# Optimization experiments

Measured on AMD Instinct MI355X. Metric: run time of the kernel, lower is better.

## Reference

```python
import jax, jax.numpy as jnp
import numpy as np

VS = VT = 32000; E = 512; H = 512; B = 32; S = 128; T = 128


def _gru_step(x, h, Wx, bx, Urz, brz, Un, bn):
    # x: [B, I], h: [B, H]
    gx = x @ Wx + bx                       # [B, 3H]
    xr, xz, xn = jnp.split(gx, 3, axis=-1)
    hrz = h @ Urz + brz                    # [B, 2H]
    hr, hz = jnp.split(hrz, 2, axis=-1)
    r = jax.nn.sigmoid(xr + hr)
    z = jax.nn.sigmoid(xz + hz)
    n = jnp.tanh(xn + (r * h) @ Un + bn)
    return (1.0 - z) * h + z * n


def setup_inputs() -> dict:
    key = jax.random.key(0)
    ks = jax.random.split(key, 24)
    s = 0.02
    f = lambda k, shape: (jax.random.normal(k, shape, dtype=jnp.float32) * s)
    return {
        "src": jax.random.randint(ks[0], (B, S), 0, VS),
        "tgt": jax.random.randint(ks[1], (B, T), 0, VT),
        "enc_embed": f(ks[2], (VS, E)),
        "enc_Wx": f(ks[3], (E, 3 * H)),
        "enc_bx": jnp.zeros((3 * H,), jnp.float32),
        "enc_Urz": f(ks[4], (H, 2 * H)),
        "enc_brz": jnp.zeros((2 * H,), jnp.float32),
        "enc_Un": f(ks[5], (H, H)),
        "enc_bn": jnp.zeros((H,), jnp.float32),
        "dec_embed": f(ks[6], (VT, E)),
        "dec_Wx": f(ks[7], (E + H, 3 * H)),
        "dec_bx": jnp.zeros((3 * H,), jnp.float32),
        "dec_Urz": f(ks[8], (H, 2 * H)),
        "dec_brz": jnp.zeros((2 * H,), jnp.float32),
        "dec_Un": f(ks[9], (H, H)),
        "dec_bn": jnp.zeros((H,), jnp.float32),
        "attn_Wh": f(ks[10], (H, H)),
        "attn_Ws": f(ks[11], (H, H)),
        "attn_v": f(ks[12], (H,)),
        "out_W": f(ks[13], (2 * H, VT)),
        "out_b": jnp.zeros((VT,), jnp.float32),
    }


def reference(src, tgt, enc_embed, enc_Wx, enc_bx, enc_Urz, enc_brz, enc_Un,
              enc_bn, dec_embed, dec_Wx, dec_bx, dec_Urz, dec_brz, dec_Un,
              dec_bn, attn_Wh, attn_Ws, attn_v, out_W, out_b):
    bs = src.shape[0]
    h0 = jnp.zeros((bs, H), dtype=enc_Wx.dtype)

    # -------- encoder: scan over src timesteps --------
    src_emb = enc_embed[src]                     # [B, S, E]

    def enc_step(h, x_t):
        h = _gru_step(x_t, h, enc_Wx, enc_bx, enc_Urz, enc_brz, enc_Un, enc_bn)
        return h, h

    h, enc_hs = jax.lax.scan(enc_step, h0, jnp.swapaxes(src_emb, 0, 1))
    enc_hs = jnp.swapaxes(enc_hs, 0, 1)          # [B, S, H]

    # precompute Wh(enc_hs), identical every decoder step
    wh_enc = enc_hs @ attn_Wh                    # [B, S, H]

    # -------- decoder: scan over tgt timesteps --------
    tgt_emb = dec_embed[tgt]                     # [B, T, E]

    def dec_step(h, emb_t):
        # Bahdanau attention
        energy = jnp.einsum('bsh,h->bs', jnp.tanh(wh_enc + (h @ attn_Ws)[:, None, :]), attn_v)
        attn = jax.nn.softmax(energy, axis=-1)   # [B, S]
        ctx = jnp.einsum('bs,bsh->bh', attn, enc_hs)
        x = jnp.concatenate([emb_t, ctx], axis=-1)   # [B, E+H]
        h = _gru_step(x, h, dec_Wx, dec_bx, dec_Urz, dec_brz, dec_Un, dec_bn)
        logits = jnp.concatenate([h, ctx], axis=-1) @ out_W + out_b
        out = jax.nn.log_softmax(logits, axis=-1)
        return h, out

    _, outputs = jax.lax.scan(dec_step, h, jnp.swapaxes(tgt_emb, 0, 1))
    return jnp.swapaxes(outputs, 0, 1)           # [B, T, VT]
```

## Files before the change

kernel.cpp:

```cpp
#include <hip/hip_runtime.h>
#include <stdint.h>

#define BATCH 32
#define SEQ   128
#define HID   512
#define VTOK  32000

typedef unsigned short u16;
typedef unsigned int   u32;
typedef unsigned long long u64;
typedef float    f32x4  __attribute__((ext_vector_type(4)));
typedef short    short8 __attribute__((ext_vector_type(8)));

__device__ __forceinline__ u16 f2bf(float f) {
    u32 u = __builtin_bit_cast(u32, f);
    return (u16)((u + 0x7FFFu + ((u >> 16) & 1u)) >> 16);
}
__device__ __forceinline__ float bf2f(u16 v) {
    u32 u = ((u32)v) << 16; return __builtin_bit_cast(float, u);
}
__device__ __forceinline__ float fexp2(float x) { return __builtin_amdgcn_exp2f(x); }
__device__ __forceinline__ float frcp(float x)  { return __builtin_amdgcn_rcpf(x); }
__device__ __forceinline__ float sigmoid_f(float x) {
    return frcp(1.f + fexp2(-1.442695040888963f * x));
}
__device__ __forceinline__ float tanh_f(float x) {
    return 1.f - 2.f * frcp(1.f + fexp2(2.885390081777927f * x));
}

__device__ __forceinline__ u32 ld_sc1_u32(const u32* p) {
    return __hip_atomic_load(p, __ATOMIC_RELAXED, __HIP_MEMORY_SCOPE_AGENT);
}
__device__ __forceinline__ void st_sc1_u32(u32* p, u32 v) {
    __hip_atomic_store(p, v, __ATOMIC_RELAXED, __HIP_MEMORY_SCOPE_AGENT);
}

__device__ __forceinline__ void ld16_async(uint4& dst, const void* p) {
    asm volatile("global_load_dwordx4 %0, %1, off sc1" : "=v"(dst) : "v"(p));
}
__device__ __forceinline__ void ld4_async(u32& dst, const void* p) {
    asm volatile("global_load_dword %0, %1, off sc1" : "=v"(dst) : "v"(p));
}
__device__ __forceinline__ void wait_vm0() {
    asm volatile("s_waitcnt vmcnt(0)" ::: "memory");
    __builtin_amdgcn_sched_barrier(0);
}

__device__ __forceinline__ void gbar32(u32* flags, u32 gen) {
    asm volatile("s_waitcnt vmcnt(0)" ::: "memory");
    __syncthreads();
    if (threadIdx.x == 0) st_sc1_u32(flags + (u32)blockIdx.x * 16, gen);
    const int i = threadIdx.x;
    if (i < 32 && i != (int)blockIdx.x) {
        while (ld_sc1_u32(flags + i * 16) < gen) {}
    }
    __syncthreads();
}


__global__ __launch_bounds__(256) void transpose_cvt(
    const float* __restrict__ src, u16* __restrict__ dst, int K, int N)
{
    __shared__ float tile[32][33];
    const int n0 = blockIdx.x * 32, k0 = blockIdx.y * 32;
    const int tx = threadIdx.x & 31, ty = threadIdx.x >> 5;
    #pragma unroll
    for (int j = 0; j < 32; j += 8)
        tile[ty + j][tx] = src[(size_t)(k0 + ty + j) * N + n0 + tx];
    __syncthreads();
    #pragma unroll
    for (int j = 0; j < 32; j += 8)
        dst[(size_t)(n0 + ty + j) * K + k0 + tx] = f2bf(tile[tx][ty + j]);
}

__global__ __launch_bounds__(256) void cvt_f32_bf16(
    const float* __restrict__ src, u16* __restrict__ dst)
{
    const size_t i = ((size_t)blockIdx.x * 256 + threadIdx.x) * 8;
    float4 v0 = *(const float4*)(src + i);
    float4 v1 = *(const float4*)(src + i + 4);
    uint4 pk;
    pk.x = (u32)f2bf(v0.x) | ((u32)f2bf(v0.y) << 16);
    pk.y = (u32)f2bf(v0.z) | ((u32)f2bf(v0.w) << 16);
    pk.z = (u32)f2bf(v1.x) | ((u32)f2bf(v1.y) << 16);
    pk.w = (u32)f2bf(v1.z) | ((u32)f2bf(v1.w) << 16);
    *(uint4*)(dst + i) = pk;
}

__global__ __launch_bounds__(128) void gather_emb_bf16(
    const int* __restrict__ idx, const float* __restrict__ emb, u16* __restrict__ out)
{
    const int r = blockIdx.x;
    const int token = idx[r];
    const int i = threadIdx.x * 4;
    float4 v = *(const float4*)(emb + (size_t)token * 512 + i);
    uint2 pk;
    pk.x = (u32)f2bf(v.x) | ((u32)f2bf(v.y) << 16);
    pk.y = (u32)f2bf(v.z) | ((u32)f2bf(v.w) << 16);
    *(uint2*)(out + (size_t)r * 512 + i) = pk;
}

__global__ __launch_bounds__(512) void init_state(u32* hg, u32* bar)
{
    const int i = blockIdx.x * 512 + threadIdx.x;
    hg[i] = 0u;
    if (blockIdx.x < 2) bar[blockIdx.x * 512 + threadIdx.x] = 0u;
}

__global__ __launch_bounds__(256) void gemm_bf16(
    const u16* __restrict__ A, const u16* __restrict__ BT,
    const float* __restrict__ bias, float* __restrict__ C,
    int M, int N, int K)
{
    __shared__ __align__(16) u16 As[128][40];
    __shared__ __align__(16) u16 Bs[128][40];
    const int tid  = threadIdx.x;
    const int lane = tid & 63, wave = tid >> 6;
    const int wm = (wave & 1) * 64, wn = (wave >> 1) * 64;
    const int lrow = lane & 15, lk = (lane >> 4) * 8;
    const int srow = tid >> 2, skof = (tid & 3) * 8;
    const size_t K_ = (size_t)K;
    const u16* Ag = A + ((size_t)blockIdx.y * 128 + srow) * K_ + skof;
    const u16* Bg = BT + ((size_t)blockIdx.x * 128 + srow) * K_ + skof;
    f32x4 acc[4][4] = {};
    for (int k0 = 0; k0 < K; k0 += 32) {
        uint4 a0 = *(const uint4*)(Ag + k0);
        uint4 a1 = *(const uint4*)(Ag + 64 * K_ + k0);
        uint4 b0 = *(const uint4*)(Bg + k0);
        uint4 b1 = *(const uint4*)(Bg + 64 * K_ + k0);
        __syncthreads();
        *(uint4*)&As[srow][skof]      = a0;
        *(uint4*)&As[srow + 64][skof] = a1;
        *(uint4*)&Bs[srow][skof]      = b0;
        *(uint4*)&Bs[srow + 64][skof] = b1;
        __syncthreads();
        short8 af[4], bf[4];
        #pragma unroll
        for (int i = 0; i < 4; ++i) af[i] = *(const short8*)&As[wm + i * 16 + lrow][lk];
        #pragma unroll
        for (int j = 0; j < 4; ++j) bf[j] = *(const short8*)&Bs[wn + j * 16 + lrow][lk];
        #pragma unroll
        for (int i = 0; i < 4; ++i)
            #pragma unroll
            for (int j = 0; j < 4; ++j)
                acc[i][j] = __builtin_amdgcn_mfma_f32_16x16x32_bf16(af[i], bf[j], acc[i][j], 0, 0, 0);
    }
    const int crow0 = blockIdx.y * 128 + wm + (lane >> 4) * 4;
    const int ccol0 = blockIdx.x * 128 + wn + (lane & 15);
    #pragma unroll
    for (int j = 0; j < 4; ++j) {
        const float bv = bias ? bias[ccol0 + j * 16] : 0.f;
        #pragma unroll
        for (int i = 0; i < 4; ++i)
            #pragma unroll
            for (int rr = 0; rr < 4; ++rr)
                C[(size_t)(crow0 + i * 16 + rr) * N + (ccol0 + j * 16)] = acc[i][j][rr] + bv;
    }
}

__global__ __launch_bounds__(512) void enc_coop(
    const float* __restrict__ gx, const u16* __restrict__ Urz, const u16* __restrict__ Un,
    const float* __restrict__ brz, const float* __restrict__ bn,
    u32* __restrict__ hg, u32* __restrict__ rhg, u32* __restrict__ zg,
    u16* __restrict__ enc_hs, u16* __restrict__ spack,
    u32* __restrict__ flags)
{
    const int w = blockIdx.x, tid = threadIdx.x;
    const int v = tid >> 6, lane = tid & 63;
    const int nl = lane & 15, kq = lane >> 4;
    __shared__ __align__(16) u16 UrzS[32][520];
    __shared__ __align__(16) u16 UnS[16][520];
    for (int idx = tid; idx < 32 * 64; idx += 512) {
        const int r = idx >> 6, c = idx & 63;
        *(uint4*)&UrzS[r][c * 8] = *(const uint4*)(Urz + (size_t)(w * 32 + r) * 512 + c * 8);
    }
    for (int idx = tid; idx < 16 * 64; idx += 512) {
        const int r = idx >> 6, c = idx & 63;
        *(uint4*)&UnS[r][c * 8] = *(const uint4*)(Un + (size_t)(w * 16 + r) * 512 + c * 8);
    }
    __syncthreads();
    for (int t = 0; t < SEQ; ++t) {
        const u32* hgA = hg + (t & 1) * 8192;
        u32*       hgW = hg + ((t + 1) & 1) * 8192;
        const u64* hq  = (const u64*)hgA;
        const u64* rq  = (const u64*)rhg;
        if (v < 4) {
            const int bt = v & 1, tl = v >> 1;
            const int n = w * 32 + tl * 16 + nl;
            const int brow = bt * 16 + nl;
            uint4 a[16]; u32 hvp[4];
            const u64* ab = hq + brow * 128 + kq * 2;
            #pragma unroll
            for (int i = 0; i < 16; ++i) ld16_async(a[i], ab + i * 8);
            #pragma unroll
            for (int rr = 0; rr < 4; ++rr)
                ld4_async(hvp[rr], hgA + (bt * 16 + kq * 4 + rr) * 256 + (n >> 1));
            float gxr_pf[4];
            #pragma unroll
            for (int rr = 0; rr < 4; ++rr) {
                const int b = bt * 16 + kq * 4 + rr;
                gxr_pf[rr] = gx[((size_t)(b * SEQ + t)) * 1536 + n];
            }
            wait_vm0();
            const u16* wl = &UrzS[tl * 16 + nl][0];
            f32x4 acc = {0.f, 0.f, 0.f, 0.f};
            #pragma unroll
            for (int i = 0; i < 16; ++i) {
                short8 bfv = *(const short8*)(wl + i * 32 + kq * 8);
                acc = __builtin_amdgcn_mfma_f32_16x16x32_bf16(
                    __builtin_bit_cast(short8, a[i]), bfv, acc, 0, 0, 0);
            }
            if (n < 512) {
                u32 pk[4];
                #pragma unroll
                for (int rr = 0; rr < 4; ++rr) {
                    const float r = sigmoid_f(gxr_pf[rr] + acc[rr] + brz[n]);
                    const float hold = bf2f((u16)((n & 1) ? (hvp[rr] >> 16) : (hvp[rr] & 0xFFFF)));
                    pk[rr] = (u32)f2bf(r * hold);
                }
                #pragma unroll
                for (int rr = 0; rr < 4; ++rr) {
                    u32 oth = (u32)__shfl_xor((int)pk[rr], 1);
                    if ((n & 1) == 0) {
                        const int b = bt * 16 + kq * 4 + rr;
                        st_sc1_u32(rhg + b * 256 + (n >> 1), (pk[rr] & 0xFFFF) | (oth << 16));
                    }
                }
            } else {
                #pragma unroll
                for (int rr = 0; rr < 4; ++rr) {
                    const int b = bt * 16 + kq * 4 + rr;
                    const float z = sigmoid_f(gxr_pf[rr] + acc[rr] + brz[n]);
                    st_sc1_u32(zg + b * 512 + (n - 512), __float_as_uint(z));
                }
            }
        }
        gbar32(flags, (u32)(2 * t + 1));
        if (v < 2) {
            const int bt = v;
            const int n = w * 16 + nl;
            const int brow = bt * 16 + nl;
            uint4 a[16]; u32 hvp[4], zvp[4];
            const u64* ab = rq + brow * 128 + kq * 2;
            #pragma unroll
            for (int i = 0; i < 16; ++i) ld16_async(a[i], ab + i * 8);
            #pragma unroll
            for (int rr = 0; rr < 4; ++rr) {
                const int b = bt * 16 + kq * 4 + rr;
                ld4_async(hvp[rr], hgA + b * 256 + (n >> 1));
                ld4_async(zvp[rr], zg + b * 512 + n);
            }
            float gxr_pf[4];
            #pragma unroll
            for (int rr = 0; rr < 4; ++rr) {
                const int b = bt * 16 + kq * 4 + rr;
                gxr_pf[rr] = gx[((size_t)(b * SEQ + t)) * 1536 + 1024 + n];
            }
            wait_vm0();
            const u16* wl = &UnS[nl][0];
            f32x4 acc = {0.f, 0.f, 0.f, 0.f};
            #pragma unroll
            for (int i = 0; i < 16; ++i) {
                short8 bfv = *(const short8*)(wl + i * 32 + kq * 8);
                acc = __builtin_amdgcn_mfma_f32_16x16x32_bf16(
                    __builtin_bit_cast(short8, a[i]), bfv, acc, 0, 0, 0);
            }
            u32 pk[4];
            #pragma unroll
            for (int rr = 0; rr < 4; ++rr) {
                const int b = bt * 16 + kq * 4 + rr;
                const float nn = tanh_f(gxr_pf[rr] + acc[rr] + bn[n]);
                const float z = __uint_as_float(zvp[rr]);
                const float hold = bf2f((u16)((n & 1) ? (hvp[rr] >> 16) : (hvp[rr] & 0xFFFF)));
                const float hn = (1.f - z) * hold + z * nn;
                const u16 hb = f2bf(hn);
                pk[rr] = (u32)hb;
                enc_hs[((size_t)(b * SEQ + t)) * 512 + n] = hb;
                spack[(((size_t)b * 16 + (t >> 3)) * 512 + n) * 8 + (t & 7)] = hb;
            }
            #pragma unroll
            for (int rr = 0; rr < 4; ++rr) {
                u32 oth = (u32)__shfl_xor((int)pk[rr], 1);
                if ((n & 1) == 0) {
                    const int b = bt * 16 + kq * 4 + rr;
                    st_sc1_u32(hgW + b * 256 + (n >> 1), (pk[rr] & 0xFFFF) | (oth << 16));
                }
            }
        }
        gbar32(flags, (u32)(2 * t + 2));
    }
}

__global__ __launch_bounds__(512) void dec_coop(
    const float* __restrict__ gxe, const u16* __restrict__ wh_bf, const u16* __restrict__ spack,
    const float* __restrict__ attn_v, const float* __restrict__ brz, const float* __restrict__ bn,
    const u16* __restrict__ Urz, const u16* __restrict__ Ws,
    const u16* __restrict__ WxC, const u16* __restrict__ Un,
    u32* __restrict__ hg, u32* __restrict__ rhg, u32* __restrict__ ctxg,
    u32* __restrict__ zg, u32* __restrict__ gg, u32* __restrict__ aWsg,
    u16* __restrict__ hctx, u32* __restrict__ flags)
{
    const int w = blockIdx.x, tid = threadIdx.x;
    const int v = tid >> 6, lane = tid & 63;
    const int nl = lane & 15, kq = lane >> 4;
    __shared__ __align__(16) u16 UWsS[48][520];
    __shared__ __align__(16) u16 WxCS[48][520];
    __shared__ __align__(16) u16 UnS2[16][520];
    __shared__ float hWsL[4 * 132], redE[512], attnL[128];
    __shared__ u16 ctxL[512];
    for (int idx = tid; idx < 48 * 64; idx += 512) {
        const int r = idx >> 6, c = idx & 63;
        const int gcol = w * 48 + r;
        const u16* s0 = (gcol < 1024 ? Urz + (size_t)gcol * 512
                                     : Ws + (size_t)(gcol - 1024) * 512) + c * 8;
        *(uint4*)&UWsS[r][c * 8] = *(const uint4*)s0;
        *(uint4*)&WxCS[r][c * 8] = *(const uint4*)(WxC + (size_t)gcol * 512 + c * 8);
    }
    for (int idx = tid; idx < 16 * 64; idx += 512) {
        const int r = idx >> 6, c = idx & 63;
        *(uint4*)&UnS2[r][c * 8] = *(const uint4*)(Un + (size_t)(w * 16 + r) * 512 + c * 8);
    }
    __syncthreads();
    for (int t = 0; t < SEQ; ++t) {
        const u32* hgA = hg + (t & 1) * 8192;
        u32*       hgW = hg + ((t + 1) & 1) * 8192;
        const u64* hq  = (const u64*)hgA;
        const u64* rq  = (const u64*)rhg;
        const u64* cq  = (const u64*)ctxg;
        f32x4 aPk = {0.f, 0.f, 0.f, 0.f};
        if (v < 6) {
            const int bt = v & 1, tl = v >> 1;
            const int n = w * 48 + tl * 16 + nl;
            const int brow = bt * 16 + nl;
            uint4 a[16];
            const u64* ab = hq + brow * 128 + kq * 2;
            #pragma unroll
            for (int i = 0; i < 16; ++i) ld16_async(a[i], ab + i * 8);
            wait_vm0();
            const u16* wl = &UWsS[tl * 16 + nl][0];
            f32x4 acc = {0.f, 0.f, 0.f, 0.f};
            #pragma unroll
            for (int i = 0; i < 16; ++i) {
                short8 bfv = *(const short8*)(wl + i * 32 + kq * 8);
                acc = __builtin_amdgcn_mfma_f32_16x16x32_bf16(
                    __builtin_bit_cast(short8, a[i]), bfv, acc, 0, 0, 0);
            }
            if (n < 1024) {
                aPk = acc;
            } else {
                #pragma unroll
                for (int rr = 0; rr < 4; ++rr) {
                    const int b = bt * 16 + kq * 4 + rr;
                    st_sc1_u32(aWsg + b * 512 + (n - 1024), __float_as_uint(acc[rr]));
                }
            }
        }
        gbar32(flags, (u32)(4 * t + 1));
        {
            const int b = w;
            {
                u32 hwv;
                ld4_async(hwv, aWsg + b * 512 + tid);
                wait_vm0();
                hWsL[(tid >> 7) * 132 + (tid & 127)] = __uint_as_float(hwv);
            }
            __syncthreads();
            {
                const int s = tid >> 2, q = tid & 3;
                const u16* whr = wh_bf + ((size_t)(b * SEQ + s)) * 512 + q * 128;
                const float* avq = attn_v + q * 128;
                const float* hwq = &hWsL[q * 132];
                float e = 0.f;
                #pragma unroll 4
                for (int i = 0; i < 128; i += 8) {
                    uint4 wv = *(const uint4*)(whr + i);
                    float4 h0 = *(const float4*)(hwq + i);
                    float4 h1 = *(const float4*)(hwq + i + 4);
                    float4 v0 = *(const float4*)(avq + i);
                    float4 v1 = *(const float4*)(avq + i + 4);
                    e += v0.x * tanh_f(bf2f((u16)(wv.x & 0xFFFF)) + h0.x)
                       + v0.y * tanh_f(bf2f((u16)(wv.x >> 16))    + h0.y)
                       + v0.z * tanh_f(bf2f((u16)(wv.y & 0xFFFF)) + h0.z)
                       + v0.w * tanh_f(bf2f((u16)(wv.y >> 16))    + h0.w)
                       + v1.x * tanh_f(bf2f((u16)(wv.z & 0xFFFF)) + h1.x)
                       + v1.y * tanh_f(bf2f((u16)(wv.z >> 16))    + h1.y)
                       + v1.z * tanh_f(bf2f((u16)(wv.w & 0xFFFF)) + h1.z)
                       + v1.w * tanh_f(bf2f((u16)(wv.w >> 16))    + h1.w);
                }
                redE[tid] = e;
            }
            __syncthreads();
            if (tid < 64) {
                float e0 = redE[4 * tid] + redE[4 * tid + 1] + redE[4 * tid + 2] + redE[4 * tid + 3];
                float e1 = redE[4 * (tid + 64)] + redE[4 * (tid + 64) + 1]
                         + redE[4 * (tid + 64) + 2] + redE[4 * (tid + 64) + 3];
                float m = fmaxf(e0, e1);
                for (int o = 32; o >= 1; o >>= 1) m = fmaxf(m, __shfl_xor(m, o));
                float p0 = fexp2((e0 - m) * 1.442695040888963f);
                float p1 = fexp2((e1 - m) * 1.442695040888963f);
                float ss = p0 + p1;
                for (int o = 32; o >= 1; o >>= 1) ss += __shfl_xor(ss, o);
                const float inv = frcp(ss);
                attnL[tid]      = p0 * inv;
                attnL[tid + 64] = p1 * inv;
            }
            __syncthreads();
            {
                const int d = tid;
                float cv = 0.f;
                const u16* sp = spack + ((size_t)b * 16 * 512 + d) * 8;
                #pragma unroll 4
                for (int sb = 0; sb < 16; ++sb) {
                    uint4 sv = *(const uint4*)(sp + (size_t)sb * 4096);
                    const float* al = &attnL[sb * 8];
                    cv += al[0] * bf2f((u16)(sv.x & 0xFFFF)) + al[1] * bf2f((u16)(sv.x >> 16))
                        + al[2] * bf2f((u16)(sv.y & 0xFFFF)) + al[3] * bf2f((u16)(sv.y >> 16))
                        + al[4] * bf2f((u16)(sv.z & 0xFFFF)) + al[5] * bf2f((u16)(sv.z >> 16))
                        + al[6] * bf2f((u16)(sv.w & 0xFFFF)) + al[7] * bf2f((u16)(sv.w >> 16));
                }
                const u16 cb = f2bf(cv);
                ctxL[d] = cb;
                hctx[((size_t)(b * SEQ + t)) * 1024 + 512 + d] = cb;
            }
            __syncthreads();
            if (tid < 256) {
                u32 pk = (u32)ctxL[2 * tid] | ((u32)ctxL[2 * tid + 1] << 16);
                st_sc1_u32(ctxg + b * 256 + tid, pk);
            }
        }
        gbar32(flags, (u32)(4 * t + 2));
        if (v < 6) {
            const int bt = v & 1, tl = v >> 1;
            const int n = w * 48 + tl * 16 + nl;
            const int brow = bt * 16 + nl;
            uint4 a[16]; u32 hvp[4];
            const u64* ab = cq + brow * 128 + kq * 2;
            #pragma unroll
            for (int i = 0; i < 16; ++i) ld16_async(a[i], ab + i * 8);
            #pragma unroll
            for (int rr = 0; rr < 4; ++rr)
                ld4_async(hvp[rr], hgA + (bt * 16 + kq * 4 + rr) * 256 + ((n & 511) >> 1));
            float gxr_pf[4];
            #pragma unroll
            for (int rr = 0; rr < 4; ++rr) {
                const int b = bt * 16 + kq * 4 + rr;
                gxr_pf[rr] = gxe[((size_t)(b * SEQ + t)) * 1536 + n];
            }
            wait_vm0();
            const u16* wl = &WxCS[tl * 16 + nl][0];
            f32x4 acc = {0.f, 0.f, 0.f, 0.f};
            #pragma unroll
            for (int i = 0; i < 16; ++i) {
                short8 bfv = *(const short8*)(wl + i * 32 + kq * 8);
                acc = __builtin_amdgcn_mfma_f32_16x16x32_bf16(
                    __builtin_bit_cast(short8, a[i]), bfv, acc, 0, 0, 0);
            }
            if (n < 512) {
                u32 pk[4];
                #pragma unroll
                for (int rr = 0; rr < 4; ++rr) {
                    const float r = sigmoid_f(gxr_pf[rr] + acc[rr] + aPk[rr] + brz[n]);
                    const float hold = bf2f((u16)((n & 1) ? (hvp[rr] >> 16) : (hvp[rr] & 0xFFFF)));
                    pk[rr] = (u32)f2bf(r * hold);
                }
                #pragma unroll
                for (int rr = 0; rr < 4; ++rr) {
                    u32 oth = (u32)__shfl_xor((int)pk[rr], 1);
                    if ((n & 1) == 0) {
                        const int b = bt * 16 + kq * 4 + rr;
                        st_sc1_u32(rhg + b * 256 + (n >> 1), (pk[rr] & 0xFFFF) | (oth << 16));
                    }
                }
            } else if (n < 1024) {
                #pragma unroll
                for (int rr = 0; rr < 4; ++rr) {
                    const int b = bt * 16 + kq * 4 + rr;
                    const float z = sigmoid_f(gxr_pf[rr] + acc[rr] + aPk[rr] + brz[n]);
                    st_sc1_u32(zg + b * 512 + (n - 512), __float_as_uint(z));
                }
            } else {
                #pragma unroll
                for (int rr = 0; rr < 4; ++rr) {
                    const int b = bt * 16 + kq * 4 + rr;
                    st_sc1_u32(gg + b * 512 + (n - 1024), __float_as_uint(gxr_pf[rr] + acc[rr]));
                }
            }
        }
        gbar32(flags, (u32)(4 * t + 3));
        if (v < 2) {
            const int bt = v;
            const int n = w * 16 + nl;
            const int brow = bt * 16 + nl;
            uint4 a[16]; u32 gvp[4], zvp[4], hvp[4];
            const u64* ab = rq + brow * 128 + kq * 2;
            #pragma unroll
            for (int i = 0; i < 16; ++i) ld16_async(a[i], ab + i * 8);
            #pragma unroll
            for (int rr = 0; rr < 4; ++rr) {
                const int b = bt * 16 + kq * 4 + rr;
                ld4_async(gvp[rr], gg + b * 512 + n);
                ld4_async(zvp[rr], zg + b * 512 + n);
                ld4_async(hvp[rr], hgA + b * 256 + (n >> 1));
            }
            wait_vm0();
            const u16* wl = &UnS2[nl][0];
            f32x4 acc = {0.f, 0.f, 0.f, 0.f};
            #pragma unroll
            for (int i = 0; i < 16; ++i) {
                short8 bfv = *(const short8*)(wl + i * 32 + kq * 8);
                acc = __builtin_amdgcn_mfma_f32_16x16x32_bf16(
                    __builtin_bit_cast(short8, a[i]), bfv, acc, 0, 0, 0);
            }
            u32 pk[4];
            #pragma unroll
            for (int rr = 0; rr < 4; ++rr) {
                const int b = bt * 16 + kq * 4 + rr;
                const float nn = tanh_f(__uint_as_float(gvp[rr]) + acc[rr] + bn[n]);
                const float z = __uint_as_float(zvp[rr]);
                const float hold = bf2f((u16)((n & 1) ? (hvp[rr] >> 16) : (hvp[rr] & 0xFFFF)));
                const float hn = (1.f - z) * hold + z * nn;
                const u16 hb = f2bf(hn);
                pk[rr] = (u32)hb;
                hctx[((size_t)(b * SEQ + t)) * 1024 + n] = hb;
            }
            #pragma unroll
            for (int rr = 0; rr < 4; ++rr) {
                u32 oth = (u32)__shfl_xor((int)pk[rr], 1);
                if ((n & 1) == 0) {
                    const int b = bt * 16 + kq * 4 + rr;
                    st_sc1_u32(hgW + b * 256 + (n >> 1), (pk[rr] & 0xFFFF) | (oth << 16));
                }
            }
        }
        gbar32(flags, (u32)(4 * t + 4));
    }
}

__global__ __launch_bounds__(256) void log_softmax_rows(float* __restrict__ out)
{
    const int row = blockIdx.x, tid = threadIdx.x;
    float* p = out + (size_t)row * VTOK;
    __shared__ float rbM[4], rbS[4];
    const float L2E = 1.442695040888963f;
    float m = -3.0e38f, s = 0.f;
    for (int i = tid * 4; i < VTOK; i += 1024) {
        float4 v = *(const float4*)(p + i);
        float lm = fmaxf(fmaxf(v.x, v.y), fmaxf(v.z, v.w));
        float nm = fmaxf(m, lm);
        s = s * fexp2((m - nm) * L2E)
          + fexp2((v.x - nm) * L2E) + fexp2((v.y - nm) * L2E)
          + fexp2((v.z - nm) * L2E) + fexp2((v.w - nm) * L2E);
        m = nm;
    }
    for (int o = 32; o >= 1; o >>= 1) {
        float om = __shfl_xor(m, o), os = __shfl_xor(s, o);
        float nm = fmaxf(m, om);
        s = s * fexp2((m - nm) * L2E) + os * fexp2((om - nm) * L2E);
        m = nm;
    }
    if ((tid & 63) == 0) { rbM[tid >> 6] = m; rbS[tid >> 6] = s; }
    __syncthreads();
    {
        float fm = fmaxf(fmaxf(rbM[0], rbM[1]), fmaxf(rbM[2], rbM[3]));
        float fs = rbS[0] * fexp2((rbM[0] - fm) * L2E) + rbS[1] * fexp2((rbM[1] - fm) * L2E)
                 + rbS[2] * fexp2((rbM[2] - fm) * L2E) + rbS[3] * fexp2((rbM[3] - fm) * L2E);
        m = fm; s = fs;
    }
    const float lse = m + __builtin_amdgcn_logf(s) * 0.6931471805599453f;
    for (int i = tid * 4; i < VTOK; i += 1024) {
        float4 v = *(const float4*)(p + i);
        v.x -= lse; v.y -= lse; v.z -= lse; v.w -= lse;
        *(float4*)(p + i) = v;
    }
}

extern "C" void kernel_launch(void* const* d_in, const int* in_sizes, int n_in,
                              void* d_out, int out_size, void* d_ws, size_t ws_size,
                              hipStream_t stream)
{
    (void)in_sizes; (void)n_in; (void)out_size; (void)ws_size;
    const int*   src       = (const int*)  d_in[0];
    const int*   tgt       = (const int*)  d_in[1];
    const float* enc_embed = (const float*)d_in[2];
    const float* enc_Wx    = (const float*)d_in[3];
    const float* enc_bx    = (const float*)d_in[4];
    const float* enc_Urz   = (const float*)d_in[5];
    const float* enc_brz   = (const float*)d_in[6];
    const float* enc_Un    = (const float*)d_in[7];
    const float* enc_bn    = (const float*)d_in[8];
    const float* dec_embed = (const float*)d_in[9];
    const float* dec_Wx    = (const float*)d_in[10];
    const float* dec_bx    = (const float*)d_in[11];
    const float* dec_Urz   = (const float*)d_in[12];
    const float* dec_brz   = (const float*)d_in[13];
    const float* dec_Un    = (const float*)d_in[14];
    const float* dec_bn    = (const float*)d_in[15];
    const float* attn_Wh   = (const float*)d_in[16];
    const float* attn_Ws   = (const float*)d_in[17];
    const float* attn_v    = (const float*)d_in[18];
    const float* out_W     = (const float*)d_in[19];
    const float* out_b     = (const float*)d_in[20];

    char* ob = (char*)d_out;
    float* gx_enc   = (float*)(ob + 0);
    float* gxe_dec  = (float*)(ob + 25165824);
    float* wh_enc   = (float*)(ob + 50331648);
    u16*   Aenc     = (u16*)(ob + 58720256);
    u16*   Adec     = (u16*)(ob + 62914560);
    u16*   enc_hs   = (u16*)(ob + 67108864);
    u16*   spack    = (u16*)(ob + 71303168);
    u16*   wh_bf    = (u16*)(ob + 75497472);
    u16*   encWxT   = (u16*)(ob + 79691776);
    u16*   decWxET  = (u16*)(ob + 81264640);
    u16*   WhT      = (u16*)(ob + 82837504);
    u16*   UrzET    = (u16*)(ob + 83361792);
    u16*   UnET     = (u16*)(ob + 84410368);
    u16*   UrzDT    = (u16*)(ob + 84934656);
    u16*   UnDT     = (u16*)(ob + 85983232);
    u16*   WsT      = (u16*)(ob + 86507520);
    u16*   WxCT     = (u16*)(ob + 87031808);
    u32*   hg       = (u32*)(ob + 88604672);
    u32*   rhg      = (u32*)(ob + 88670208);
    u32*   ctxg     = (u32*)(ob + 88702976);
    u32*   zg       = (u32*)(ob + 88735744);
    u32*   gg       = (u32*)(ob + 88801280);
    u32*   aWsg     = (u32*)(ob + 88866816);
    u32*   barp     = (u32*)(ob + 88932352);

    char* wb = (char*)d_ws;
    u16* outWT = (u16*)(wb + 0);
    u16* hctx  = (u16*)(wb + 65536000);

    transpose_cvt<<<dim3(48, 16),   256, 0, stream>>>(enc_Wx,  encWxT, 512, 1536);
    transpose_cvt<<<dim3(48, 16),   256, 0, stream>>>(dec_Wx,  decWxET,512, 1536);
    transpose_cvt<<<dim3(16, 16),   256, 0, stream>>>(attn_Wh, WhT,    512, 512);
    transpose_cvt<<<dim3(1000, 32), 256, 0, stream>>>(out_W,   outWT, 1024, 32000);
    transpose_cvt<<<dim3(32, 16),   256, 0, stream>>>(enc_Urz, UrzET,  512, 1024);
    transpose_cvt<<<dim3(16, 16),   256, 0, stream>>>(enc_Un,  UnET,   512, 512);
    transpose_cvt<<<dim3(32, 16),   256, 0, stream>>>(dec_Urz, UrzDT,  512, 1024);
    transpose_cvt<<<dim3(16, 16),   256, 0, stream>>>(dec_Un,  UnDT,   512, 512);
    transpose_cvt<<<dim3(16, 16),   256, 0, stream>>>(attn_Ws, WsT,    512, 512);
    transpose_cvt<<<dim3(48, 16),   256, 0, stream>>>(dec_Wx + (size_t)512 * 1536, WxCT, 512, 1536);
    gather_emb_bf16<<<4096, 128, 0, stream>>>(src, enc_embed, Aenc);
    gather_emb_bf16<<<4096, 128, 0, stream>>>(tgt, dec_embed, Adec);

    gemm_bf16<<<dim3(12, 32), 256, 0, stream>>>(Aenc, encWxT,  enc_bx, gx_enc,  4096, 1536, 512);
    gemm_bf16<<<dim3(12, 32), 256, 0, stream>>>(Adec, decWxET, dec_bx, gxe_dec, 4096, 1536, 512);

    init_state<<<32, 512, 0, stream>>>(hg, barp);

    {
        u32* encF = barp;
        void* args[] = { (void*)&gx_enc, (void*)&UrzET, (void*)&UnET, (void*)&enc_brz,
                         (void*)&enc_bn, (void*)&hg, (void*)&rhg, (void*)&zg,
                         (void*)&enc_hs, (void*)&spack, (void*)&encF };
        hipLaunchCooperativeKernel((void*)enc_coop, dim3(32), dim3(512), args, 0, stream);
    }

    gemm_bf16<<<dim3(4, 32), 256, 0, stream>>>(enc_hs, WhT, nullptr, wh_enc, 4096, 512, 512);
    cvt_f32_bf16<<<1024, 256, 0, stream>>>(wh_enc, wh_bf);

    {
        u32* decF = barp + 512;
        void* args[] = { (void*)&gxe_dec, (void*)&wh_bf, (void*)&spack, (void*)&attn_v,
                         (void*)&dec_brz, (void*)&dec_bn, (void*)&UrzDT, (void*)&WsT,
                         (void*)&WxCT, (void*)&UnDT, (void*)&hg, (void*)&rhg, (void*)&ctxg,
                         (void*)&zg, (void*)&gg, (void*)&aWsg, (void*)&hctx, (void*)&decF };
        hipLaunchCooperativeKernel((void*)dec_coop, dim3(32), dim3(512), args, 0, stream);
    }

    gemm_bf16<<<dim3(250, 32), 256, 0, stream>>>(hctx, outWT, out_b, (float*)d_out, 4096, VTOK, 1024);
    log_softmax_rows<<<4096, 256, 0, stream>>>((float*)d_out);
}
```

Before: 5.437 ms.

## Overlap output-projection GEMM with decoder recurrence via extra cooperative blocks

Launches the decoder cooperative kernel with 96 extra blocks that pull 128x128 output-GEMM tiles from an atomic counter. Each tile waits on a progress flag that the decoder raises once the hidden/context rows for that block of timesteps are ready. hctx is now laid out time-major so finished rows form contiguous tiles, and the GEMM epilogue permutes rows back to batch-major. The decoder also reads a bf16, time-major repack of its input-gate projections. This aims to hide most of the large vocabulary GEMM under the latency-bound recurrence, but the extra blocks compete with the recurrent blocks for memory bandwidth and may slow the grid barriers. Buffers are relocated into workspace when it is large enough, otherwise it falls back to the old separate GEMM.

```diff
diff --git a/kernel.cpp b/kernel.cpp
--- a/kernel.cpp
+++ b/kernel.cpp
@@ -5,6 +5,7 @@
 #define SEQ   128
 #define HID   512
 #define VTOK  32000
+#define NTILES 8000
 
 typedef unsigned short u16;
 typedef unsigned int   u32;
@@ -87,6 +88,24 @@
     *(uint4*)(dst + i) = pk;
 }
 
+__global__ __launch_bounds__(192) void repack_gxe(
+    const float* __restrict__ src, u16* __restrict__ dst)
+{
+    const int r = blockIdx.x;
+    const int b = r >> 7, t = r & 127;
+    const float* s = src + (size_t)r * 1536;
+    u16* d = dst + ((size_t)(t * 32 + b)) * 1536;
+    const int i = threadIdx.x * 8;
+    float4 v0 = *(const float4*)(s + i);
+    float4 v1 = *(const float4*)(s + i + 4);
+    uint4 pk;
+    pk.x = (u32)f2bf(v0.x) | ((u32)f2bf(v0.y) << 16);
+    pk.y = (u32)f2bf(v0.z) | ((u32)f2bf(v0.w) << 16);
+    pk.z = (u32)f2bf(v1.x) | ((u32)f2bf(v1.y) << 16);
+    pk.w = (u32)f2bf(v1.z) | ((u32)f2bf(v1.w) << 16);
+    *(uint4*)(d + i) = pk;
+}
+
 __global__ __launch_bounds__(128) void gather_emb_bf16(
     const int* __restrict__ idx, const float* __restrict__ emb, u16* __restrict__ out)
 {
@@ -100,17 +119,17 @@
     *(uint2*)(out + (size_t)r * 512 + i) = pk;
 }
 
-__global__ __launch_bounds__(512) void init_state(u32* hg, u32* bar)
+__global__ __launch_bounds__(512) void init_state(u32* hg, u32* ctrl)
 {
     const int i = blockIdx.x * 512 + threadIdx.x;
     hg[i] = 0u;
-    if (blockIdx.x < 2) bar[blockIdx.x * 512 + threadIdx.x] = 0u;
+    if (blockIdx.x < 4) ctrl[blockIdx.x * 512 + threadIdx.x] = 0u;
 }
 
 __global__ __launch_bounds__(256) void gemm_bf16(
     const u16* __restrict__ A, const u16* __restrict__ BT,
     const float* __restrict__ bias, float* __restrict__ C,
-    int M, int N, int K)
+    int M, int N, int K, int rperm)
 {
     __shared__ __align__(16) u16 As[128][40];
     __shared__ __align__(16) u16 Bs[128][40];
@@ -153,8 +172,73 @@
         #pragma unroll
         for (int i = 0; i < 4; ++i)
             #pragma unroll
-            for (int rr = 0; rr < 4; ++rr)
-                C[(size_t)(crow0 + i * 16 + rr) * N + (ccol0 + j * 16)] = acc[i][j][rr] + bv;
+            for (int rr = 0; rr < 4; ++rr) {
+                int r = crow0 + i * 16 + rr;
+                int orow = rperm ? ((r & 31) * 128 + (r >> 5)) : r;
+                C[(size_t)orow * N + (ccol0 + j * 16)] = acc[i][j][rr] + bv;
+            }
+    }
+}
+
+__device__ __forceinline__ void gemm_tiles(
+    const u16* __restrict__ hctx, const u16* __restrict__ outWT,
+    const float* __restrict__ out_b, float* __restrict__ C,
+    u32* progress, u32* tctr, u16* lds, u32* wslot)
+{
+    const int tid = threadIdx.x;
+    u16* As = lds;
+    u16* Bs = lds + 5120;
+    const int lane = tid & 63, wave = tid >> 6;
+    const int wm = (wave & 1) * 64, wn = (wave >> 1) * 32;
+    const int lrow = lane & 15, lk = (lane >> 4) * 8;
+    const int srow = tid >> 2, skof = (tid & 3) * 8;
+    for (;;) {
+        if (tid == 0) *wslot = __hip_atomic_fetch_add(tctr, 1u, __ATOMIC_RELAXED, __HIP_MEMORY_SCOPE_AGENT);
+        __syncthreads();
+        const u32 k = *wslot;
+        __syncthreads();
+        if (k >= (u32)NTILES) break;
+        const int rt = (int)(k / 250u), ct = (int)(k % 250u);
+        if (tid == 0) {
+            while (ld_sc1_u32(progress) < (u32)((rt + 1) * 4)) __builtin_amdgcn_s_sleep(8);
+        }
+        __syncthreads();
+        const u16* Ag = hctx + ((size_t)(rt * 128 + srow)) * 1024 + skof;
+        const u16* Bg = outWT + ((size_t)(ct * 128 + srow)) * 1024 + skof;
+        f32x4 acc[4][2] = {};
+        for (int k0 = 0; k0 < 1024; k0 += 32) {
+            uint4 a0; ld16_async(a0, Ag + k0);
+            uint4 b0 = *(const uint4*)(Bg + k0);
+            wait_vm0();
+            __syncthreads();
+            *(uint4*)&As[srow * 40 + skof] = a0;
+            *(uint4*)&Bs[srow * 40 + skof] = b0;
+            __syncthreads();
+            short8 af[4], bf[2];
+            #pragma unroll
+            for (int i = 0; i < 4; ++i) af[i] = *(const short8*)&As[(wm + i * 16 + lrow) * 40 + lk];
+            #pragma unroll
+            for (int j = 0; j < 2; ++j) bf[j] = *(const short8*)&Bs[(wn + j * 16 + lrow) * 40 + lk];
+            #pragma unroll
+            for (int i = 0; i < 4; ++i)
+                #pragma unroll
+                for (int j = 0; j < 2; ++j)
+                    acc[i][j] = __builtin_amdgcn_mfma_f32_16x16x32_bf16(af[i], bf[j], acc[i][j], 0, 0, 0);
+        }
+        const int crow0 = rt * 128 + wm + (lane >> 4) * 4;
+        const int ccol0 = ct * 128 + wn + (lane & 15);
+        #pragma unroll
+        for (int j = 0; j < 2; ++j) {
+            const float bv = out_b[ccol0 + j * 16];
+            #pragma unroll
+            for (int i = 0; i < 4; ++i)
+                #pragma unroll
+                for (int rr = 0; rr < 4; ++rr) {
+                    int r = crow0 + i * 16 + rr;
+                    int orow = (r & 31) * 128 + (r >> 5);
+                    C[(size_t)orow * VTOK + (ccol0 + j * 16)] = acc[i][j][rr] + bv;
+                }
+        }
     }
 }
 
@@ -292,13 +376,15 @@
 }
 
 __global__ __launch_bounds__(512) void dec_coop(
-    const float* __restrict__ gxe, const u16* __restrict__ wh_bf, const u16* __restrict__ spack,
+    const u16* __restrict__ gxe_bf, const u16* __restrict__ wh_bf, const u16* __restrict__ spack,
     const float* __restrict__ attn_v, const float* __restrict__ brz, const float* __restrict__ bn,
     const u16* __restrict__ Urz, const u16* __restrict__ Ws,
     const u16* __restrict__ WxC, const u16* __restrict__ Un,
     u32* __restrict__ hg, u32* __restrict__ rhg, u32* __restrict__ ctxg,
     u32* __restrict__ zg, u32* __restrict__ gg, u32* __restrict__ aWsg,
-    u16* __restrict__ hctx, u32* __restrict__ flags)
+    u16* __restrict__ hctx, u32* __restrict__ flags,
+    const u16* __restrict__ outWT, const float* __restrict__ out_b, float* __restrict__ Cout,
+    u32* __restrict__ progress, u32* __restrict__ tctr, int do_gemm)
 {
     const int w = blockIdx.x, tid = threadIdx.x;
     const int v = tid >> 6, lane = tid & 63;
@@ -308,6 +394,12 @@
     __shared__ __align__(16) u16 UnS2[16][520];
     __shared__ float hWsL[4 * 132], redE[512], attnL[128];
     __shared__ u16 ctxL[512];
+    __shared__ u32 wslotS;
+    if (w >= 32) {
+        if (do_gemm)
+            gemm_tiles(hctx, outWT, out_b, Cout, progress, tctr, &UWsS[0][0], &wslotS);
+        return;
+    }
     for (int idx = tid; idx < 48 * 64; idx += 512) {
         const int r = idx >> 6, c = idx & 63;
         const int gcol = w * 48 + r;
@@ -418,14 +510,13 @@
                         + al[4] * bf2f((u16)(sv.z & 0xFFFF)) + al[5] * bf2f((u16)(sv.z >> 16))
                         + al[6] * bf2f((u16)(sv.w & 0xFFFF)) + al[7] * bf2f((u16)(sv.w >> 16));
                 }
-                const u16 cb = f2bf(cv);
-                ctxL[d] = cb;
-                hctx[((size_t)(b * SEQ + t)) * 1024 + 512 + d] = cb;
+                ctxL[d] = f2bf(cv);
             }
             __syncthreads();
             if (tid < 256) {
                 u32 pk = (u32)ctxL[2 * tid] | ((u32)ctxL[2 * tid + 1] << 16);
                 st_sc1_u32(ctxg + b * 256 + tid, pk);
+                st_sc1_u32((u32*)(hctx + ((size_t)(t * 32 + b)) * 1024 + 512) + tid, pk);
             }
         }
         gbar32(flags, (u32)(4 * t + 2));
@@ -444,7 +535,7 @@
             #pragma unroll
             for (int rr = 0; rr < 4; ++rr) {
                 const int b = bt * 16 + kq * 4 + rr;
-                gxr_pf[rr] = gxe[((size_t)(b * SEQ + t)) * 1536 + n];
+                gxr_pf[rr] = bf2f(gxe_bf[((size_t)(t * 32 + b)) * 1536 + n]);
             }
             wait_vm0();
             const u16* wl = &WxCS[tl * 16 + nl][0];
@@ -519,21 +610,24 @@
                 const float z = __uint_as_float(zvp[rr]);
                 const float hold = bf2f((u16)((n & 1) ? (hvp[rr] >> 16) : (hvp[rr] & 0xFFFF)));
                 const float hn = (1.f - z) * hold + z * nn;
-                const u16 hb = f2bf(hn);
-                pk[rr] = (u32)hb;
-                hctx[((size_t)(b * SEQ + t)) * 1024 + n] = hb;
+                pk[rr] = (u32)f2bf(hn);
             }
             #pragma unroll
             for (int rr = 0; rr < 4; ++rr) {
                 u32 oth = (u32)__shfl_xor((int)pk[rr], 1);
                 if ((n & 1) == 0) {
                     const int b = bt * 16 + kq * 4 + rr;
-                    st_sc1_u32(hgW + b * 256 + (n >> 1), (pk[rr] & 0xFFFF) | (oth << 16));
+                    const u32 pr = (pk[rr] & 0xFFFF) | (oth << 16);
+                    st_sc1_u32(hgW + b * 256 + (n >> 1), pr);
+                    st_sc1_u32((u32*)(hctx + ((size_t)(t * 32 + b)) * 1024 + n), pr);
                 }
             }
         }
         gbar32(flags, (u32)(4 * t + 4));
-    }
+        if (do_gemm && w == 0 && tid == 0) st_sc1_u32(progress, (u32)(t + 1));
+    }
+    if (do_gemm)
+        gemm_tiles(hctx, outWT, out_b, Cout, progress, tctr, &UWsS[0][0], &wslotS);
 }
 
 __global__ __launch_bounds__(256) void log_softmax_rows(float* __restrict__ out)
@@ -578,7 +672,7 @@
                               void* d_out, int out_size, void* d_ws, size_t ws_size,
                               hipStream_t stream)
 {
-    (void)in_sizes; (void)n_in; (void)out_size; (void)ws_size;
+    (void)in_sizes; (void)n_in; (void)out_size;
     const int*   src       = (const int*)  d_in[0];
     const int*   tgt       = (const int*)  d_in[1];
     const float* enc_embed = (const float*)d_in[2];
@@ -603,33 +697,49 @@
 
     char* ob = (char*)d_out;
     float* gx_enc   = (float*)(ob + 0);
-    float* gxe_dec  = (float*)(ob + 25165824);
+    float* gxe_f32  = (float*)(ob + 25165824);
     float* wh_enc   = (float*)(ob + 50331648);
     u16*   Aenc     = (u16*)(ob + 58720256);
     u16*   Adec     = (u16*)(ob + 62914560);
     u16*   enc_hs   = (u16*)(ob + 67108864);
-    u16*   spack    = (u16*)(ob + 71303168);
-    u16*   wh_bf    = (u16*)(ob + 75497472);
-    u16*   encWxT   = (u16*)(ob + 79691776);
-    u16*   decWxET  = (u16*)(ob + 81264640);
-    u16*   WhT      = (u16*)(ob + 82837504);
-    u16*   UrzET    = (u16*)(ob + 83361792);
-    u16*   UnET     = (u16*)(ob + 84410368);
-    u16*   UrzDT    = (u16*)(ob + 84934656);
-    u16*   UnDT     = (u16*)(ob + 85983232);
-    u16*   WsT      = (u16*)(ob + 86507520);
-    u16*   WxCT     = (u16*)(ob + 87031808);
-    u32*   hg       = (u32*)(ob + 88604672);
-    u32*   rhg      = (u32*)(ob + 88670208);
-    u32*   ctxg     = (u32*)(ob + 88702976);
-    u32*   zg       = (u32*)(ob + 88735744);
-    u32*   gg       = (u32*)(ob + 88801280);
-    u32*   aWsg     = (u32*)(ob + 88866816);
-    u32*   barp     = (u32*)(ob + 88932352);
+    u16*   encWxT   = (u16*)(ob + 71303168);
+    u16*   decWxET  = (u16*)(ob + 72876032);
+    u16*   WhT      = (u16*)(ob + 74448896);
+    u16*   UrzET    = (u16*)(ob + 74973184);
+    u16*   UnET     = (u16*)(ob + 76021760);
+    u16*   UrzDT    = (u16*)(ob + 76546048);
+    u16*   UnDT     = (u16*)(ob + 77594624);
+    u16*   WsT      = (u16*)(ob + 78118912);
+    u16*   WxCT     = (u16*)(ob + 78643200);
+    u16*   gxe_bf   = (u16*)(ob + 511705088);
 
     char* wb = (char*)d_ws;
-    u16* outWT = (u16*)(wb + 0);
-    u16* hctx  = (u16*)(wb + 65536000);
+    u16*  outWT = (u16*)(wb + 0);
+    u16*  hctx  = (u16*)(wb + 65536000);
+    const size_t NEED = 82649088;
+    const int overlap = (ws_size >= NEED) ? 1 : 0;
+
+    u16 *wh_bf, *spack; u32 *comm;
+    if (overlap) {
+        wh_bf = (u16*)(wb + 73924608);
+        spack = (u16*)(wb + 78118912);
+        comm  = (u32*)(wb + 82313216);
+    } else {
+        comm  = (u32*)(ob + 80216064);
+        wh_bf = (u16*)(ob + 80551936);
+        spack = (u16*)(ob + 84746240);
+    }
+    u32* hgp  = comm;
+    u32* ctrl = comm + 16384;
+    u32* encF = ctrl;
+    u32* decF = ctrl + 512;
+    u32* prog = ctrl + 1024;
+    u32* tctr = ctrl + 1040;
+    u32* rhg  = comm + 18432;
+    u32* ctxg = comm + 26624;
+    u32* zg   = comm + 34816;
+    u32* gg   = comm + 51200;
+    u32* aWsg = comm + 67584;
 
     transpose_cvt<<<dim3(48, 16),   256, 0, stream>>>(enc_Wx,  encWxT, 512, 1536);
     transpose_cvt<<<dim3(48, 16),   256, 0, stream>>>(dec_Wx,  decWxET,512, 1536);
@@ -644,31 +754,38 @@
     gather_emb_bf16<<<4096, 128, 0, stream>>>(src, enc_embed, Aenc);
     gather_emb_bf16<<<4096, 128, 0, stream>>>(tgt, dec_embed, Adec);
 
-    gemm_bf16<<<dim3(12, 32), 256, 0, stream>>>(Aenc, encWxT,  enc_bx, gx_enc,  4096, 1536, 512);
-    gemm_bf16<<<dim3(12, 32), 256, 0, stream>>>(Adec, decWxET, dec_bx, gxe_dec, 4096, 1536, 512);
-
-    init_state<<<32, 512, 0, stream>>>(hg, barp);
+    gemm_bf16<<<dim3(12, 32), 256, 0, stream>>>(Aenc, encWxT,  enc_bx, gx_enc,  4096, 1536, 512, 0);
+    gemm_bf16<<<dim3(12, 32), 256, 0, stream>>>(Adec, decWxET, dec_bx, gxe_f32, 4096, 1536, 512, 0);
+    repack_gxe<<<4096, 192, 0, stream>>>(gxe_f32, gxe_bf);
+
+    init_state<<<32, 512, 0, stream>>>(hgp, ctrl);
 
     {
-        u32* encF = barp;
         void* args[] = { (void*)&gx_enc, (void*)&UrzET, (void*)&UnET, (void*)&enc_brz,
-                         (void*)&enc_bn, (void*)&hg, (void*)&rhg, (void*)&zg,
+                         (void*)&enc_bn, (void*)&hgp, (void*)&rhg, (void*)&zg,
                          (void*)&enc_hs, (void*)&spack, (void*)&encF };
         hipLaunchCooperativeKernel((void*)enc_coop, dim3(32), dim3(512), args, 0, stream);
     }
 
-    gemm_bf16<<<dim3(4, 32), 256, 0, stream>>>(enc_hs, WhT, nullptr, wh_enc, 4096, 512, 512);
+    gemm_bf16<<<dim3(4, 32), 256, 0, stream>>>(enc_hs, WhT, nullptr, wh_enc, 4096, 512, 512, 0);
     cvt_f32_bf16<<<1024, 256, 0, stream>>>(wh_enc, wh_bf);
 
     {
-        u32* decF = barp + 512;
-        void* args[] = { (void*)&gxe_dec, (void*)&wh_bf, (void*)&spack, (void*)&attn_v,
+        float* Cout = (float*)d_out;
+        int do_gemm = overlap;
+        void* args[] = { (void*)&gxe_bf, (void*)&wh_bf, (void*)&spack, (void*)&attn_v,
                          (void*)&dec_brz, (void*)&dec_bn, (void*)&UrzDT, (void*)&WsT,
-                         (void*)&WxCT, (void*)&UnDT, (void*)&hg, (void*)&rhg, (void*)&ctxg,
-                         (void*)&zg, (void*)&gg, (void*)&aWsg, (void*)&hctx, (void*)&decF };
-        hipLaunchCooperativeKernel((void*)dec_coop, dim3(32), dim3(512), args, 0, stream);
-    }
-
-    gemm_bf16<<<dim3(250, 32), 256, 0, stream>>>(hctx, outWT, out_b, (float*)d_out, 4096, VTOK, 1024);
+                         (void*)&WxCT, (void*)&UnDT, (void*)&hgp, (void*)&rhg, (void*)&ctxg,
+                         (void*)&zg, (void*)&gg, (void*)&aWsg, (void*)&hctx, (void*)&decF,
+                         (void*)&outWT, (void*)&out_b, (void*)&Cout,
+                         (void*)&prog, (void*)&tctr, (void*)&do_gemm };
+        hipLaunchCooperativeKernel((void*)dec_coop, dim3(overlap ? 128 : 32), dim3(512),
+                                   args, 0, stream);
+    }
+
+    if (!overlap)
+        gemm_bf16<<<dim3(250, 32), 256, 0, stream>>>(hctx, outWT, out_b, (float*)d_out,
+                                                     4096, VTOK, 1024, 1);
+
     log_softmax_rows<<<4096, 256, 0, stream>>>((float*)d_out);
 }
```

Result: faster. 5.167 ms (-5.0%).
